# Optimization experiments

Hardware: AMD Instinct MI355X
Metric: run time of the kernel (lower is better)

The kernel has to match this reference:

```python
import jax, jax.numpy as jnp
import numpy as np

HEIGHT = 0.1        # height_factor
MIN_DIST = 10       # min_distance
PROM = 0.05         # prominence_factor


def _find_peaks(xn):
    """scipy.signal.find_peaks(xn, height=HEIGHT, distance=MIN_DIST,
    prominence=PROM) for a single 1D signal, vectorized.
    (Plateau handling omitted: for continuous random inputs exact ties have
    probability zero, so strict local maxima match scipy's _local_maxima_1d.)"""
    N = xn.shape[0]
    pos = jnp.arange(N)

    # 1) strict local maxima (endpoints can never be peaks in scipy)
    interior = (xn[1:-1] > xn[:-2]) & (xn[1:-1] > xn[2:])
    is_peak = jnp.pad(interior, (1, 1), constant_values=False)

    # 2) height filter
    cand = is_peak & (xn >= HEIGHT)

    # 3) distance-based greedy suppression: highest peak first, remove
    #    neighbors with |i-j| < MIN_DIST (matches _select_by_peak_distance)
    order = jnp.argsort(-xn)  # descending by value

    def step(suppressed, idx):
        keep_this = cand[idx] & ~suppressed[idx]
        near = (jnp.abs(pos - idx) < MIN_DIST) & (pos != idx)
        suppressed = suppressed | (keep_this & near)
        return suppressed, keep_this

    _, keeps = jax.lax.scan(step, jnp.zeros(N, dtype=bool), order)
    keep = jnp.zeros(N, dtype=bool).at[order].set(keeps)

    # 4) prominence (wlen=None -> full-signal base search, per position):
    #    left base  = min x over (L, i] where L = last j<i with x[j] > x[i]
    #    right base = min x over [i, R) where R = first j>i with x[j] > x[i]
    greater = xn[None, :] > xn[:, None]              # [i, j]: x_j > x_i
    left_stop = greater & (pos[None, :] < pos[:, None])
    L = jnp.max(jnp.where(left_stop, pos[None, :], -1), axis=1)
    right_stop = greater & (pos[None, :] > pos[:, None])
    R = jnp.min(jnp.where(right_stop, pos[None, :], N), axis=1)

    big = jnp.asarray(jnp.inf, xn.dtype)
    in_l = (pos[None, :] > L[:, None]) & (pos[None, :] <= pos[:, None])
    lmin = jnp.min(jnp.where(in_l, xn[None, :], big), axis=1)
    in_r = (pos[None, :] >= pos[:, None]) & (pos[None, :] < R[:, None])
    rmin = jnp.min(jnp.where(in_r, xn[None, :], big), axis=1)
    prominence = xn - jnp.maximum(lmin, rmin)

    keep = keep & (prominence >= PROM)
    return keep.astype(xn.dtype)


def setup_inputs() -> dict:
    key = jax.random.key(0)
    x = jax.random.normal(key, (16, 2048), dtype=jnp.float32)
    return {"x": x}


def reference(x):
    # per-sample min-max normalization, as in the torch module
    xmin = jnp.min(x, axis=-1, keepdims=True)
    xmax = jnp.max(x, axis=-1, keepdims=True)
    xn = (x - xmin) / (xmax - xmin + 1e-5)
    return jax.vmap(_find_peaks)(xn)
```

## Files before the change

### kernel.cpp

```cpp
#include <hip/hip_runtime.h>

#define N 2048
#define NT 256
#define EL 8
#define HEIGHTF 0.1f
#define PROMF 0.05f
#define MD1 9
#define LVLS 8
#define ACT_G 20
#define ACT_SZ 3136

__global__ __launch_bounds__(NT)
void peak_kernel(const float* __restrict__ x, float* __restrict__ out) {
    __shared__ float xs[N];
    __shared__ float act[ACT_SZ];
    __shared__ unsigned int nk32[2 + NT + 3];
    __shared__ float TMX[LVLS][N];
    __shared__ float TMN[LVLS][N];
    __shared__ float wred[8];
    __shared__ int cont[2];
    __shared__ int kcnt;
    __shared__ unsigned short klist[NT];
    __shared__ unsigned char keepres[N];

    const int row = blockIdx.x;
    const int t = threadIdx.x;
    const int base = t * EL;
    const int abase = ACT_G + t * 12;
    const float* xr = x + row * (size_t)N;

    float4 Ld0 = ((const float4*)(xr + base))[0];
    float4 Ld1 = ((const float4*)(xr + base))[1];
    float v0[EL] = {Ld0.x, Ld0.y, Ld0.z, Ld0.w, Ld1.x, Ld1.y, Ld1.z, Ld1.w};
    float mn = v0[0], mx = v0[0];
    #pragma unroll
    for (int e = 1; e < EL; ++e) { mn = fminf(mn, v0[e]); mx = fmaxf(mx, v0[e]); }
    #pragma unroll
    for (int off = 32; off > 0; off >>= 1) {
        mn = fminf(mn, __shfl_xor(mn, off, 64));
        mx = fmaxf(mx, __shfl_xor(mx, off, 64));
    }
    const int wv = t >> 6, ln = t & 63;
    if (ln == 0) { wred[wv] = mn; wred[4 + wv] = mx; }
    if (t == 0) {
        nk32[0] = 0; nk32[1] = 0; nk32[2+NT] = 0; nk32[2+NT+1] = 0; nk32[2+NT+2] = 0;
        cont[0] = 0; kcnt = 0;
    }
    if (t < ACT_G) act[t] = -1e30f;
    if (t < 48) act[3088 + t] = -1e30f;
    __syncthreads();
    const float xmin = fminf(fminf(wred[0], wred[1]), fminf(wred[2], wred[3]));
    const float xmax = fmaxf(fmaxf(wred[4], wred[5]), fmaxf(wred[6], wred[7]));
    const float den = (xmax - xmin) + 1e-5f;
    float vn[EL];
    #pragma unroll
    for (int e = 0; e < EL; ++e) {
        vn[e] = (v0[e] - xmin) / den;
        xs[base + e] = vn[e];
    }
    __syncthreads();

    unsigned int undec = 0, kept = 0;
    #pragma unroll
    for (int e = 0; e < EL; ++e) {
        int i = base + e;
        float v = vn[e];
        float lf = (e == 0) ? ((i >= 1) ? xs[i-1] : 3e38f) : vn[e-1];
        float rt = (e == EL-1) ? ((i+1 < N) ? xs[i+1] : 3e38f) : vn[e+1];
        bool c = (i >= 1) && (i <= N-2) && (v > lf) && (v > rt) && (v >= HEIGHTF);
        if (c) undec |= (1u << e);
        act[abase + e] = c ? v : -1e30f;
    }
    __syncthreads();

    unsigned int* nkp = nk32 + 2;
    for (int round = 0; round < 2048; ++round) {
        unsigned int winb = 0;
        if (undec) {
            const float* ab = act + abase;
            float4 r0 = *(const float4*)(ab - 20);
            float4 r1 = *(const float4*)(ab - 12);
            float4 r2 = *(const float4*)(ab - 8);
            float4 r3 = *(const float4*)(ab + 0);
            float4 r4 = *(const float4*)(ab + 4);
            float4 r5 = *(const float4*)(ab + 12);
            float4 r6 = *(const float4*)(ab + 16);
            float4 r7 = *(const float4*)(ab + 24);
            float a[32] = {r0.x,r0.y,r0.z,r0.w, r1.x,r1.y,r1.z,r1.w,
                           r2.x,r2.y,r2.z,r2.w, r3.x,r3.y,r3.z,r3.w,
                           r4.x,r4.y,r4.z,r4.w, r5.x,r5.y,r5.z,r5.w,
                           r6.x,r6.y,r6.z,r6.w, r7.x,r7.y,r7.z,r7.w};
            #pragma unroll
            for (int e = 0; e < EL; ++e) {
                if (undec & (1u << e)) {
                    float v = vn[e];
                    float wl = -1e30f, wr = -1e30f;
                    #pragma unroll
                    for (int d = 0; d < MD1; ++d) wl = fmaxf(wl, a[e + 3 + d]);
                    #pragma unroll
                    for (int d = 0; d < MD1; ++d) wr = fmaxf(wr, a[e + 13 + d]);
                    if (wl < v && wr <= v) winb |= (1u << e);
                }
            }
        }
        nkp[t] = winb;
        __syncthreads();
        if (undec) {
            unsigned long long W = 0;
            #pragma unroll
            for (int q = 0; q < 5; ++q)
                W |= ((unsigned long long)(nkp[t - 2 + q] & 0xFFu)) << (8 * q);
            #pragma unroll
            for (int e = 0; e < EL; ++e) {
                if (undec & (1u << e)) {
                    unsigned long long w19 = (W >> (e + 7)) & 0x7FFFFULL;
                    if ((w19 >> MD1) & 1ULL) {
                        kept |= (1u << e);
                        undec &= ~(1u << e);
                        act[abase + e] = -1e30f;
                    } else if (w19 & ~(1ULL << MD1)) {
                        undec &= ~(1u << e);
                        act[abase + e] = -1e30f;
                    }
                }
            }
        }
        if (t == 0) cont[(round + 1) & 1] = 0;
        if (undec) cont[round & 1] = 1;
        __syncthreads();
        if (cont[round & 1] == 0) break;
    }

    #pragma unroll
    for (int e = 0; e < EL; ++e) {
        keepres[base + e] = 0;
        if (kept & (1u << e)) {
            int slot = atomicAdd(&kcnt, 1);
            klist[slot] = (unsigned short)(base + e);
        }
    }

    float cx[EL], cn[EL];
    #pragma unroll
    for (int j = 0; j < EL; ++j) {
        int i = t + j * NT;
        float a0 = xs[i];
        bool inb = (i + 1 < N);
        float nb = inb ? xs[i + 1] : 0.0f;
        cx[j] = fmaxf(a0, inb ? nb : -3e38f);
        cn[j] = fminf(a0, inb ? nb : 3e38f);
        TMX[0][i] = cx[j];
        TMN[0][i] = cn[j];
    }
    __syncthreads();
    for (int Lv = 1; Lv < LVLS; ++Lv) {
        int h = 1 << Lv;
        #pragma unroll
        for (int j = 0; j < EL; ++j) {
            int i = t + j * NT;
            bool inb = (i + h < N);
            float bx = inb ? TMX[Lv-1][i+h] : -3e38f;
            float bn = inb ? TMN[Lv-1][i+h] : 3e38f;
            cx[j] = fmaxf(cx[j], bx);
            cn[j] = fminf(cn[j], bn);
            TMX[Lv][i] = cx[j];
            TMN[Lv][i] = cn[j];
        }
        __syncthreads();
    }

    if (t < kcnt) {
        const int i = klist[t];
        const float v = xs[i];
        float m = v;
        int p = i - 1;
        while (p >= 0) {
            int len = p + 1;
            int k = (len >= (1 << LVLS)) ? LVLS : (31 - __clz(len));
            int s = p + 1 - (1 << k);
            float wmx = (k == 0) ? xs[s] : TMX[k-1][s];
            if (wmx > v) {
                while (k > 0) {
                    int half = 1 << (k - 1);
                    int rs = s + half;
                    float rm = (k == 1) ? xs[rs] : TMX[k-2][rs];
                    if (rm > v) s = rs;
                    else m = fminf(m, (k == 1) ? xs[rs] : TMN[k-2][rs]);
                    --k;
                }
                break;
            } else {
                m = fminf(m, (k == 0) ? xs[s] : TMN[k-1][s]);
                p = s - 1;
            }
        }
        const float lmin = m;
        m = v;
        p = i + 1;
        while (p < N) {
            int len = N - p;
            int k = (len >= (1 << LVLS)) ? LVLS : (31 - __clz(len));
            float wmx = (k == 0) ? xs[p] : TMX[k-1][p];
            if (wmx > v) {
                while (k > 0) {
                    int half = 1 << (k - 1);
                    float lm = (k == 1) ? xs[p] : TMX[k-2][p];
                    if (!(lm > v)) {
                        m = fminf(m, (k == 1) ? xs[p] : TMN[k-2][p]);
                        p += half;
                    }
                    --k;
                }
                break;
            } else {
                m = fminf(m, (k == 0) ? xs[p] : TMN[k-1][p]);
                p += 1 << k;
            }
        }
        const float rmin = m;
        if (v - fmaxf(lmin, rmin) >= PROMF) keepres[i] = 1;
    }
    __syncthreads();

    float res[EL];
    #pragma unroll
    for (int e = 0; e < EL; ++e) res[e] = keepres[base + e] ? 1.0f : 0.0f;
    float* outr = out + row * (size_t)N + base;
    ((float4*)outr)[0] = make_float4(res[0], res[1], res[2], res[3]);
    ((float4*)outr)[1] = make_float4(res[4], res[5], res[6], res[7]);
}

extern "C" void kernel_launch(void* const* d_in, const int* in_sizes, int n_in,
                              void* d_out, int out_size, void* d_ws, size_t ws_size,
                              hipStream_t stream) {
    const float* x = (const float*)d_in[0];
    float* outp = (float*)d_out;
    const int rows = in_sizes[0] / N;
    peak_kernel<<<rows, NT, 0, stream>>>(x, outp);
}
```

Baseline: 26.19 us.

## Keep suppression window in registers and cut a barrier per greedy round

The distance-suppression loop now loads the candidate window once into a 40-element register array and updates it locally from neighbours' win bitmasks, so the shared act buffer is no longer rewritten. Each round needs only one barrier instead of two, and the window max uses a shared doubling tree (pairs, quads, eights). The atomicAdd-based compaction of kept peaks is replaced by a wave prefix scan plus per-wave totals, which is merged into an existing barrier. Register pressure rises from the 40-float array and the intermediate max arrays, which could lower occupancy.

```diff
diff --git a/kernel.cpp b/kernel.cpp
--- a/kernel.cpp
+++ b/kernel.cpp
@@ -7,27 +7,25 @@
 #define PROMF 0.05f
 #define MD1 9
 #define LVLS 8
-#define ACT_G 20
-#define ACT_SZ 3136
 
 __global__ __launch_bounds__(NT)
 void peak_kernel(const float* __restrict__ x, float* __restrict__ out) {
     __shared__ float xs[N];
-    __shared__ float act[ACT_SZ];
-    __shared__ unsigned int nk32[2 + NT + 3];
+    __shared__ float actl[16 + N + 24];
+    __shared__ unsigned int nk32[3 + NT + 3];
     __shared__ float TMX[LVLS][N];
     __shared__ float TMN[LVLS][N];
     __shared__ float wred[8];
     __shared__ int cont[2];
-    __shared__ int kcnt;
+    __shared__ int wtot[4];
     __shared__ unsigned short klist[NT];
     __shared__ unsigned char keepres[N];
 
     const int row = blockIdx.x;
     const int t = threadIdx.x;
     const int base = t * EL;
-    const int abase = ACT_G + t * 12;
     const float* xr = x + row * (size_t)N;
+    const int wv = t >> 6, ln = t & 63;
 
     float4 Ld0 = ((const float4*)(xr + base))[0];
     float4 Ld1 = ((const float4*)(xr + base))[1];
@@ -40,15 +38,16 @@
         mn = fminf(mn, __shfl_xor(mn, off, 64));
         mx = fmaxf(mx, __shfl_xor(mx, off, 64));
     }
-    const int wv = t >> 6, ln = t & 63;
     if (ln == 0) { wred[wv] = mn; wred[4 + wv] = mx; }
     if (t == 0) {
-        nk32[0] = 0; nk32[1] = 0; nk32[2+NT] = 0; nk32[2+NT+1] = 0; nk32[2+NT+2] = 0;
-        cont[0] = 0; kcnt = 0;
-    }
-    if (t < ACT_G) act[t] = -1e30f;
-    if (t < 48) act[3088 + t] = -1e30f;
-    __syncthreads();
+        nk32[0] = 0; nk32[1] = 0; nk32[2] = 0;
+        nk32[3+NT] = 0; nk32[3+NT+1] = 0; nk32[3+NT+2] = 0;
+        cont[0] = 0;
+    }
+    if (t < 16) actl[t] = -1e30f;
+    if (t < 24) actl[16 + N + t] = -1e30f;
+    __syncthreads();
+
     const float xmin = fminf(fminf(wred[0], wred[1]), fminf(wred[2], wred[3]));
     const float xmax = fmaxf(fmaxf(wred[4], wred[5]), fmaxf(wred[6], wred[7]));
     const float den = (xmax - xmin) + 1e-5f;
@@ -69,75 +68,71 @@
         float rt = (e == EL-1) ? ((i+1 < N) ? xs[i+1] : 3e38f) : vn[e+1];
         bool c = (i >= 1) && (i <= N-2) && (v > lf) && (v > rt) && (v >= HEIGHTF);
         if (c) undec |= (1u << e);
-        act[abase + e] = c ? v : -1e30f;
-    }
-    __syncthreads();
-
-    unsigned int* nkp = nk32 + 2;
+        actl[16 + i] = c ? v : -1e30f;
+    }
+    __syncthreads();
+
+    float a[40];
+    {
+        const float4* ap = (const float4*)(actl + base);
+        #pragma unroll
+        for (int q = 0; q < 10; ++q) {
+            float4 w = ap[q];
+            a[4*q+0] = w.x; a[4*q+1] = w.y; a[4*q+2] = w.z; a[4*q+3] = w.w;
+        }
+    }
+
+    auto compute_wins = [&](unsigned int ud) -> unsigned int {
+        float m2v[25], m4v[23], m8v[19];
+        #pragma unroll
+        for (int s = 0; s < 25; ++s) m2v[s] = fmaxf(a[7+s], a[8+s]);
+        #pragma unroll
+        for (int s = 0; s < 23; ++s) m4v[s] = fmaxf(m2v[s], m2v[s+2]);
+        #pragma unroll
+        for (int s = 0; s < 19; ++s) m8v[s] = fmaxf(m4v[s], m4v[s+4]);
+        unsigned int wb = 0;
+        #pragma unroll
+        for (int e = 0; e < EL; ++e) {
+            if (ud & (1u << e)) {
+                float v = a[16+e];
+                float wl = fmaxf(m8v[e], a[15+e]);
+                float wr = fmaxf(m8v[10+e], a[25+e]);
+                if (wl < v && wr <= v) wb |= (1u << e);
+            }
+        }
+        return wb;
+    };
+
+    unsigned int winb = undec ? compute_wins(undec) : 0u;
+
+    unsigned int* nkp = nk32 + 3;
     for (int round = 0; round < 2048; ++round) {
-        unsigned int winb = 0;
-        if (undec) {
-            const float* ab = act + abase;
-            float4 r0 = *(const float4*)(ab - 20);
-            float4 r1 = *(const float4*)(ab - 12);
-            float4 r2 = *(const float4*)(ab - 8);
-            float4 r3 = *(const float4*)(ab + 0);
-            float4 r4 = *(const float4*)(ab + 4);
-            float4 r5 = *(const float4*)(ab + 12);
-            float4 r6 = *(const float4*)(ab + 16);
-            float4 r7 = *(const float4*)(ab + 24);
-            float a[32] = {r0.x,r0.y,r0.z,r0.w, r1.x,r1.y,r1.z,r1.w,
-                           r2.x,r2.y,r2.z,r2.w, r3.x,r3.y,r3.z,r3.w,
-                           r4.x,r4.y,r4.z,r4.w, r5.x,r5.y,r5.z,r5.w,
-                           r6.x,r6.y,r6.z,r6.w, r7.x,r7.y,r7.z,r7.w};
-            #pragma unroll
-            for (int e = 0; e < EL; ++e) {
-                if (undec & (1u << e)) {
-                    float v = vn[e];
-                    float wl = -1e30f, wr = -1e30f;
-                    #pragma unroll
-                    for (int d = 0; d < MD1; ++d) wl = fmaxf(wl, a[e + 3 + d]);
-                    #pragma unroll
-                    for (int d = 0; d < MD1; ++d) wr = fmaxf(wr, a[e + 13 + d]);
-                    if (wl < v && wr <= v) winb |= (1u << e);
-                }
-            }
-        }
         nkp[t] = winb;
-        __syncthreads();
-        if (undec) {
-            unsigned long long W = 0;
-            #pragma unroll
-            for (int q = 0; q < 5; ++q)
-                W |= ((unsigned long long)(nkp[t - 2 + q] & 0xFFu)) << (8 * q);
-            #pragma unroll
-            for (int e = 0; e < EL; ++e) {
-                if (undec & (1u << e)) {
-                    unsigned long long w19 = (W >> (e + 7)) & 0x7FFFFULL;
-                    if ((w19 >> MD1) & 1ULL) {
-                        kept |= (1u << e);
-                        undec &= ~(1u << e);
-                        act[abase + e] = -1e30f;
-                    } else if (w19 & ~(1ULL << MD1)) {
-                        undec &= ~(1u << e);
-                        act[abase + e] = -1e30f;
-                    }
-                }
-            }
-        }
         if (t == 0) cont[(round + 1) & 1] = 0;
         if (undec) cont[round & 1] = 1;
         __syncthreads();
         if (cont[round & 1] == 0) break;
-    }
-
-    #pragma unroll
-    for (int e = 0; e < EL; ++e) {
-        keepres[base + e] = 0;
-        if (kept & (1u << e)) {
-            int slot = atomicAdd(&kcnt, 1);
-            klist[slot] = (unsigned short)(base + e);
-        }
+        unsigned long long V = 0;
+        #pragma unroll
+        for (int q = 0; q < 7; ++q)
+            V |= ((unsigned long long)(nkp[t - 3 + q] & 0xFFu)) << (8 * q);
+        V <<= 1;
+        if (__ballot(V != 0ULL)) {
+            #pragma unroll
+            for (int e = 0; e < EL; ++e) {
+                if (undec & (1u << e)) {
+                    unsigned int w19 = (unsigned int)((V >> (16 + e)) & 0x7FFFFULL);
+                    if (w19 & (1u << 9)) { kept |= (1u << e); undec &= ~(1u << e); }
+                    else if (w19)        { undec &= ~(1u << e); }
+                }
+            }
+            #pragma unroll
+            for (int s = 0; s < 40; ++s) {
+                if ((V >> s) & 0x7FFFFULL) a[s] = -1e30f;
+            }
+        }
+        winb = 0;
+        if (__ballot(undec != 0)) winb = compute_wins(undec);
     }
 
     float cx[EL], cn[EL];
@@ -152,7 +147,28 @@
         TMX[0][i] = cx[j];
         TMN[0][i] = cn[j];
     }
-    __syncthreads();
+    int myc = __popc(kept);
+    int pre = myc;
+    #pragma unroll
+    for (int off = 1; off < 64; off <<= 1) {
+        int up = __shfl_up(pre, off, 64);
+        if (ln >= off) pre += up;
+    }
+    if (ln == 63) wtot[wv] = pre;
+    #pragma unroll
+    for (int e = 0; e < EL; ++e) keepres[base + e] = 0;
+    __syncthreads();
+
+    {
+        int woff = 0;
+        #pragma unroll
+        for (int w = 0; w < 4; ++w) woff += (w < wv) ? wtot[w] : 0;
+        int slot = woff + pre - myc;
+        #pragma unroll
+        for (int e = 0; e < EL; ++e)
+            if (kept & (1u << e)) klist[slot++] = (unsigned short)(base + e);
+    }
+    const int ktot = wtot[0] + wtot[1] + wtot[2] + wtot[3];
     for (int Lv = 1; Lv < LVLS; ++Lv) {
         int h = 1 << Lv;
         #pragma unroll
@@ -169,7 +185,7 @@
         __syncthreads();
     }
 
-    if (t < kcnt) {
+    if (t < ktot) {
         const int i = klist[t];
         const float v = xs[i];
         float m = v;
```

Measured after the change: 24.26 us. -7.4%, faster.
